# Kernel tuning notes

Measured on AMD Instinct MI355X. Metric: run time of the kernel, lower is better.

Reference implementation:

```python
import jax, jax.numpy as jnp
import numpy as np

N_NODES = 50000
N_EDGES = 600000
N_MOL = 512
N_ATOM_FEAT = 30   # NUMBER_ATOMIC_GRAPH_FEATURES
N_BOND_FEAT = 10   # NUMBER_BOND_GRAPH_FEATURES


def _sh(v):
    # Real solid spherical harmonics l=0..3, e3nn 'component' normalization
    # (sum_m Y_lm^2 = (2l+1) r^{2l}), normalize=False -> homogeneous polynomials.
    x, y, z = v[..., 0], v[..., 1], v[..., 2]
    r2 = x * x + y * y + z * z
    s3, s5, s15, s105 = 3 ** 0.5, 5 ** 0.5, 15 ** 0.5, 105 ** 0.5
    s70_4, s42_4, s7_2, s105_2 = 70 ** 0.5 / 4, 42 ** 0.5 / 4, 7 ** 0.5 / 2, 105 ** 0.5 / 2
    return jnp.stack([
        jnp.ones_like(x),                                               # l=0
        s3 * x, s3 * y, s3 * z,                                         # l=1
        s15 * x * y, s15 * y * z, 0.5 * s5 * (3 * z * z - r2),
        s15 * x * z, 0.5 * s15 * (x * x - y * y),                       # l=2
        s70_4 * y * (3 * x * x - y * y), s105 * x * y * z,
        s42_4 * y * (5 * z * z - r2), s7_2 * z * (5 * z * z - 3 * r2),
        s42_4 * x * (5 * z * z - r2), s105_2 * z * (x * x - y * y),
        s70_4 * x * (x * x - 3 * y * y),                                # l=3 (no TP path uses it)
    ], axis=-1)


def setup_inputs() -> dict:
    key = jax.random.key(0)
    ks = jax.random.split(key, 12)
    positions = jax.random.normal(ks[0], (N_NODES, 3), jnp.float32)
    x = jax.random.normal(ks[1], (N_NODES, N_ATOM_FEAT), jnp.float32)
    edge_attr = jax.random.normal(ks[2], (N_EDGES, N_BOND_FEAT), jnp.float32)
    edge_src = jax.random.randint(ks[3], (N_EDGES,), 0, N_NODES)
    edge_dst = jax.random.randint(ks[4], (N_EDGES,), 0, N_NODES)
    batch = jnp.sort(jax.random.randint(ks[5], (N_NODES,), 0, N_MOL))
    # tp1: FullyConnectedTensorProduct(30x0e, sh) -> live outputs 64x0e + 24x1o + 16x2e
    W1_0 = jax.random.normal(ks[6], (N_ATOM_FEAT, 64), jnp.float32)
    W1_1 = jax.random.normal(ks[7], (N_ATOM_FEAT, 24), jnp.float32)
    W1_2 = jax.random.normal(ks[8], (N_ATOM_FEAT, 16), jnp.float32)
    # tp2: paths 0e*0e, 1o*1o, 2e*2e -> 1x0e
    W2_0 = jax.random.normal(ks[9], (64,), jnp.float32)
    W2_1 = jax.random.normal(ks[10], (24,), jnp.float32)
    W2_2 = jax.random.normal(ks[11], (16,), jnp.float32)
    return dict(positions=positions, x=x, edge_attr=edge_attr,
                W1_0=W1_0, W1_1=W1_1, W1_2=W1_2,
                W2_0=W2_0, W2_1=W2_1, W2_2=W2_2,
                edge_src=edge_src, edge_dst=edge_dst, batch=batch)


def _forward(positions, x, edge_attr, W1_0, W1_1, W1_2, W2_0, W2_1, W2_2,
             edge_src, edge_dst, batch):
    E = edge_src.shape[0]
    seg = jax.ops.segment_sum
    edge_vec = positions[edge_src] - positions[edge_dst]            # [E,3]
    sh = _sh(edge_vec)                                              # [E,16]
    # mul_edges TP: only bond channel 0 has instructions; path_weight sqrt(2l+1)
    # cancels w3j(0,l,l)=I/sqrt(2l+1) exactly -> plain product.
    ea = edge_attr[:, :1] * sh
    ea0, ea1, ea2 = ea[:, 0:1], ea[:, 1:4], ea[:, 4:9]              # l=3 slice unused (no path)
    deg = seg(jnp.ones((E,), sh.dtype), edge_dst, num_segments=N_NODES)
    inv_sqrt_deg = jnp.where(deg > 0, jax.lax.rsqrt(jnp.maximum(deg, 1.0)), 0.0)[:, None]
    # tp1: 0e x l -> l ; path_weight*w3j collapses to 1/sqrt(fan_in=30)
    W1 = jnp.concatenate([W1_0, W1_1, W1_2], axis=1)                # [30,104]
    a = (x[edge_src] @ W1) * (1.0 / np.sqrt(N_ATOM_FEAT))           # [E,104]
    a0, a1, a2 = a[:, :64], a[:, 64:88], a[:, 88:104]
    e_feat = jnp.concatenate([
        a0 * ea0,                                                   # [E,64]  0e
        (a1[:, :, None] * ea1[:, None, :]).reshape(E, 72),          # [E,24*3] 1o
        (a2[:, :, None] * ea2[:, None, :]).reshape(E, 80),          # [E,16*5] 2e
    ], axis=1)                                                      # [E,216]
    n = seg(e_feat, edge_dst, num_segments=N_NODES) * inv_sqrt_deg  # [N,216]
    # tp2: l x l -> 0e, w3j(l,l,0)=I/sqrt(2l+1), path_weight = 1/sqrt(104)
    g = n[edge_src]                                                 # [E,216]
    t0 = (g[:, :64] * ea0) @ W2_0
    t1 = jnp.einsum('eum,em,u->e', g[:, 64:136].reshape(E, 24, 3), ea1, W2_1)
    t2 = jnp.einsum('eum,em,u->e', g[:, 136:216].reshape(E, 16, 5), ea2, W2_2)
    out_e = (t0 + t1 / np.sqrt(3.0) + t2 / np.sqrt(5.0)) * (1.0 / np.sqrt(104.0))
    node = seg(out_e[:, None], edge_dst, num_segments=N_NODES) * inv_sqrt_deg  # [N,1]
    acc = seg(node, batch, num_segments=N_MOL)                      # [M,1]
    atoms = seg(jnp.ones((N_NODES,), node.dtype), batch, num_segments=N_MOL)[:, None]
    return acc * jnp.where(atoms > 0, jax.lax.rsqrt(jnp.maximum(atoms, 1.0)), 0.0)


def reference(positions, x, edge_attr, W1_0, W1_1, W1_2, W2_0, W2_1, W2_2,
              edge_src, edge_dst, batch):
    return _forward(positions, x, edge_attr, W1_0, W1_1, W1_2,
                    W2_0, W2_1, W2_2, edge_src, edge_dst, batch)
```

## Files before the change

### kernel.cpp

```cpp
#include <hip/hip_runtime.h>

#define DEV_INLINE __device__ __forceinline__
#define MAXDEG 48

static DEV_INLINE void sh_l012(float xx, float yy, float zz, float sh[9]) {
    const float s3  = 1.7320508075688772f;
    const float s5  = 2.23606797749979f;
    const float s15 = 3.872983346207417f;
    float r2 = xx * xx + yy * yy + zz * zz;
    sh[0] = 1.0f;
    sh[1] = s3 * xx;
    sh[2] = s3 * yy;
    sh[3] = s3 * zz;
    sh[4] = s15 * xx * yy;
    sh[5] = s15 * yy * zz;
    sh[6] = 0.5f * s5 * (3.0f * zz * zz - r2);
    sh[7] = s15 * xx * zz;
    sh[8] = 0.5f * s15 * (xx * xx - yy * yy);
}

__global__ void k_prep(const float* __restrict__ x,
                       const float* __restrict__ pos,
                       const float* __restrict__ W1_0, const float* __restrict__ W1_1,
                       const float* __restrict__ W1_2, const float* __restrict__ W2_0,
                       const float* __restrict__ W2_1, const float* __restrict__ W2_2,
                       const int* __restrict__ esrc, const int* __restrict__ edst,
                       const float* __restrict__ eattr, const int* __restrict__ batch,
                       float4* __restrict__ node1, float2* __restrict__ node2,
                       int* __restrict__ deg, int2* __restrict__ rec,
                       int* __restrict__ atoms,
                       int n_nodes, int n_edges) {
    __shared__ float ws[90];
    __shared__ int hist[512];
    int t = threadIdx.x;
    int g = blockIdx.x * blockDim.x + t;
    int dst = -1, src_v = 0;
    float ea = 0.f;
    if (g < n_edges) {
        dst = edst[g];
        src_v = esrc[g];
        ea = eattr[(size_t)g * 10];
    }
    bool nodeBlock = (blockIdx.x * blockDim.x) < n_nodes;
    if (nodeBlock) {
        const float inv_s30 = 0.18257418583505536f;
        if (t < 30) {
            float s = 0.f;
            for (int u = 0; u < 64; u++) s += W1_0[t * 64 + u] * W2_0[u];
            ws[t] = s * inv_s30;
        } else if (t < 60) {
            int k = t - 30;
            float s = 0.f;
            for (int u = 0; u < 24; u++) s += W1_1[k * 24 + u] * W2_1[u];
            ws[t] = s * inv_s30;
        } else if (t < 90) {
            int k = t - 60;
            float s = 0.f;
            for (int u = 0; u < 16; u++) s += W1_2[k * 16 + u] * W2_2[u];
            ws[t] = s * inv_s30;
        }
        hist[t] = 0;
        hist[t + 256] = 0;
        __syncthreads();
        if (g < n_nodes) {
            const float* xv = x + (size_t)g * 30;
            float s0 = 0.f, s1 = 0.f, s2 = 0.f;
#pragma unroll
            for (int k = 0; k < 30; k++) {
                float xk = xv[k];
                s0 += xk * ws[k];
                s1 += xk * ws[30 + k];
                s2 += xk * ws[60 + k];
            }
            node1[g] = make_float4(pos[g * 3 + 0], pos[g * 3 + 1], pos[g * 3 + 2], s0);
            node2[g] = make_float2(s1, s2);
        }
        int v0 = blockIdx.x * 256;
        int molFirst = batch[min(v0, n_nodes - 1)];
        if (g < n_nodes) atomicAdd(&hist[batch[g] - molFirst], 1);
        __syncthreads();
        int vend = min(v0 + 255, n_nodes - 1);
        int molLast = batch[vend];
        for (int m = t; m <= molLast - molFirst; m += 256)
            if (hist[m] > 0) atomicAdd(atoms + molFirst + m, hist[m]);
    }
    if (dst >= 0) {
        int r = atomicAdd(deg + dst, 1);
        if (r < MAXDEG) rec[dst * MAXDEG + r] = make_int2(src_v, __float_as_int(ea));
    }
}

__global__ void k_passA(const float4* __restrict__ node1, const float2* __restrict__ node2,
                        const int2* __restrict__ rec, const int* __restrict__ deg,
                        float4* __restrict__ Pkg, float* __restrict__ out,
                        int n_nodes, int n_mol) {
    int g = blockIdx.x * blockDim.x + threadIdx.x;
    if (g < n_mol) out[g] = 0.f;
    int v = g >> 4, r = g & 15;
    if (v >= n_nodes) return;
    int d = min(deg[v], MAXDEG);
    const int2* row = rec + (size_t)v * MAXDEG;
    float4 pv = node1[v];
    float acc[9];
#pragma unroll
    for (int m = 0; m < 9; m++) acc[m] = 0.f;
    for (int i = r; i < d; i += 16) {
        int2 rcd = row[i];
        int src = rcd.x;
        float ea = __int_as_float(rcd.y);
        float4 n1 = node1[src];
        float2 n2 = node2[src];
        float dx = n1.x - pv.x, dy = n1.y - pv.y, dz = n1.z - pv.z;
        float sh[9];
        sh_l012(dx, dy, dz, sh);
        acc[0] += ea * n1.w;
#pragma unroll
        for (int m = 1; m < 4; m++) acc[m] += ea * sh[m] * n2.x;
#pragma unroll
        for (int m = 4; m < 9; m++) acc[m] += ea * sh[m] * n2.y;
    }
#pragma unroll
    for (int off = 1; off < 16; off <<= 1)
#pragma unroll
        for (int m = 0; m < 9; m++) acc[m] += __shfl_xor(acc[m], off);
    if (r == 0) {
        float s = (d > 0) ? rsqrtf((float)d) : 0.f;
        float4* o = Pkg + (size_t)v * 3;
        o[0] = make_float4(acc[0] * s, acc[1] * s, acc[2] * s, acc[3] * s);
        o[1] = make_float4(acc[4] * s, acc[5] * s, acc[6] * s, acc[7] * s);
        o[2] = make_float4(acc[8] * s, pv.x, pv.y, pv.z);
    }
}

__global__ void k_passB(const float4* __restrict__ node1, const float4* __restrict__ Pkg,
                        const int2* __restrict__ rec, const int* __restrict__ deg,
                        const int* __restrict__ batch, const int* __restrict__ atoms,
                        float* __restrict__ out, int n_nodes) {
    __shared__ float smol[512];
    int t = threadIdx.x;
    smol[t] = 0.f;
    smol[t + 256] = 0.f;
    __syncthreads();
    int g = blockIdx.x * blockDim.x + t;
    int v = g >> 4, r = g & 15;
    int v0 = blockIdx.x * 16;
    const float i3 = 0.5773502691896258f;
    const float i5 = 0.4472135954999579f;
    const float i104 = 0.09805806756909202f;
    int molFirst = batch[min(v0, n_nodes - 1)];
    if (v < n_nodes) {
        int d = min(deg[v], MAXDEG);
        const int2* row = rec + (size_t)v * MAXDEG;
        float4 pv = node1[v];
        float s = 0.f;
        for (int i = r; i < d; i += 16) {
            int2 rcd = row[i];
            int src = rcd.x;
            float ea = __int_as_float(rcd.y);
            const float4* Ps = Pkg + (size_t)src * 3;
            float4 p03 = Ps[0];
            float4 p47 = Ps[1];
            float4 p8p = Ps[2];
            float dx = p8p.y - pv.x, dy = p8p.z - pv.y, dz = p8p.w - pv.z;
            float sh[9];
            sh_l012(dx, dy, dz, sh);
            float t1 = sh[1] * p03.y + sh[2] * p03.z + sh[3] * p03.w;
            float t2 = sh[4] * p47.x + sh[5] * p47.y + sh[6] * p47.z + sh[7] * p47.w + sh[8] * p8p.x;
            s += ea * (p03.x + t1 * i3 + t2 * i5);
        }
#pragma unroll
        for (int off = 1; off < 16; off <<= 1) s += __shfl_xor(s, off);
        if (r == 0) {
            float isd = (d > 0) ? rsqrtf((float)d) : 0.f;
            atomicAdd(&smol[batch[v] - molFirst], s * i104 * isd);
        }
    }
    __syncthreads();
    if (v0 < n_nodes) {
        int vend = min(v0 + 15, n_nodes - 1);
        int nm = batch[vend] - molFirst + 1;
        for (int m = t; m < nm; m += 256) {
            float val = smol[m];
            if (val != 0.f) {
                int a = atoms[molFirst + m];
                float inv = (a > 0) ? rsqrtf((float)a) : 0.f;
                atomicAdd(out + molFirst + m, val * inv);
            }
        }
    }
}

extern "C" void kernel_launch(void* const* d_in, const int* in_sizes, int n_in,
                              void* d_out, int out_size, void* d_ws, size_t ws_size,
                              hipStream_t stream) {
    const float* pos   = (const float*)d_in[0];
    const float* x     = (const float*)d_in[1];
    const float* eattr = (const float*)d_in[2];
    const float* W1_0  = (const float*)d_in[3];
    const float* W1_1  = (const float*)d_in[4];
    const float* W1_2  = (const float*)d_in[5];
    const float* W2_0  = (const float*)d_in[6];
    const float* W2_1  = (const float*)d_in[7];
    const float* W2_2  = (const float*)d_in[8];
    const int* esrc  = (const int*)d_in[9];
    const int* edst  = (const int*)d_in[10];
    const int* batch = (const int*)d_in[11];

    const int n_edges = in_sizes[9];
    const int n_nodes = in_sizes[11];
    const int n_mol   = out_size;
    float* out = (float*)d_out;

    const int BS = 256;
    const int NB = (n_nodes + BS - 1) / BS;
    const int EB1 = (n_edges + BS - 1) / BS;
    const int VB16 = (16 * n_nodes + BS - 1) / BS;
    const int GRID1 = (EB1 > NB) ? EB1 : NB;

    char* ws = (char*)d_ws;
    size_t off = 0;
    auto carve = [&](size_t bytes) {
        size_t o = off;
        off = (off + bytes + 255) & ~(size_t)255;
        return o;
    };
    size_t off_deg    = carve((size_t)n_nodes * sizeof(int));
    size_t off_atoms  = carve((size_t)n_mol * sizeof(int));
    size_t zero_bytes = off;
    size_t off_n1     = carve((size_t)n_nodes * sizeof(float4));
    size_t off_n2     = carve((size_t)n_nodes * sizeof(float2));
    size_t off_Pkg    = carve((size_t)n_nodes * 3 * sizeof(float4));
    size_t off_rec    = carve((size_t)n_nodes * MAXDEG * sizeof(int2));
    (void)ws_size;

    int*    deg    = (int*)(ws + off_deg);
    int*    atoms  = (int*)(ws + off_atoms);
    float4* node1  = (float4*)(ws + off_n1);
    float2* node2  = (float2*)(ws + off_n2);
    float4* Pkg    = (float4*)(ws + off_Pkg);
    int2*   rec    = (int2*)(ws + off_rec);

    hipMemsetAsync(d_ws, 0, zero_bytes, stream);

    k_prep<<<GRID1, BS, 0, stream>>>(x, pos, W1_0, W1_1, W1_2, W2_0, W2_1, W2_2,
                                     esrc, edst, eattr, batch,
                                     node1, node2, deg, rec, atoms,
                                     n_nodes, n_edges);
    k_passA<<<VB16, BS, 0, stream>>>(node1, node2, rec, deg, Pkg, out, n_nodes, n_mol);
    k_passB<<<VB16, BS, 0, stream>>>(node1, Pkg, rec, deg, batch, atoms, out, n_nodes);
}
```

Before: 147.2 us.

## Fuse three kernels into one persistent kernel with grid-wide atomic barriers

Replaces the prep, passA and passB launches with a single persistent kernel. It is sized to occupancy times CU count, capped at 2048 blocks, and separates its phases with a software grid barrier built on an atomic counter. Per-molecule atom counts now come from a binary search over the sorted batch array, replacing the shared-memory histogram and atomics. The aim is to remove launch gaps and tail effects between kernels. In exchange it adds spin-barrier overhead, depends on every block being co-resident, and lowers parallelism in the gather passes because threads loop over the work with a grid stride.

```diff
diff --git a/kernel.cpp b/kernel.cpp
--- a/kernel.cpp
+++ b/kernel.cpp
@@ -19,8 +19,192 @@
     sh[8] = 0.5f * s15 * (xx * xx - yy * yy);
 }
 
-__global__ void k_prep(const float* __restrict__ x,
-                       const float* __restrict__ pos,
+static DEV_INLINE int lower_bound_i(const int* __restrict__ a, int n, int key) {
+    int lo = 0, hi = n;
+    while (lo < hi) {
+        int mid = (lo + hi) >> 1;
+        if (a[mid] < key) lo = mid + 1; else hi = mid;
+    }
+    return lo;
+}
+
+static DEV_INLINE void gbar(int* cnt, int nblocks, int phase) {
+    __threadfence();
+    __syncthreads();
+    if (threadIdx.x == 0) {
+        atomicAdd(cnt, 1);
+        const int target = nblocks * phase;
+        int guard = 0;
+        while (atomicAdd(cnt, 0) < target) {
+            __builtin_amdgcn_s_sleep(2);
+            if (++guard > (1 << 27)) break;
+        }
+    }
+    __syncthreads();
+    __threadfence();
+}
+
+__global__ __launch_bounds__(256, 4)
+void k_fused(const float* __restrict__ x, const float* __restrict__ pos,
+             const float* __restrict__ W1_0, const float* __restrict__ W1_1,
+             const float* __restrict__ W1_2, const float* __restrict__ W2_0,
+             const float* __restrict__ W2_1, const float* __restrict__ W2_2,
+             const int* __restrict__ esrc, const int* __restrict__ edst,
+             const float* __restrict__ eattr, const int* __restrict__ batch,
+             float4* __restrict__ node1, float2* __restrict__ node2,
+             int* __restrict__ deg, int2* __restrict__ rec,
+             float* __restrict__ atomsInv, float4* __restrict__ Pkg,
+             float* __restrict__ out, int* __restrict__ barcnt,
+             int n_nodes, int n_edges, int n_mol, int nblocks) {
+    __shared__ float ws[90];
+    __shared__ float smol[512];
+    const int t = threadIdx.x;
+    const int b = blockIdx.x;
+    const int g = b * 256 + t;
+    const int gsz = gridDim.x * 256;
+
+    {
+        const float inv_s30 = 0.18257418583505536f;
+        if (t < 30) {
+            float s = 0.f;
+            for (int u = 0; u < 64; u++) s += W1_0[t * 64 + u] * W2_0[u];
+            ws[t] = s * inv_s30;
+        } else if (t < 60) {
+            int k = t - 30;
+            float s = 0.f;
+            for (int u = 0; u < 24; u++) s += W1_1[k * 24 + u] * W2_1[u];
+            ws[t] = s * inv_s30;
+        } else if (t < 90) {
+            int k = t - 60;
+            float s = 0.f;
+            for (int u = 0; u < 16; u++) s += W1_2[k * 16 + u] * W2_2[u];
+            ws[t] = s * inv_s30;
+        }
+        __syncthreads();
+        for (int v = g; v < n_nodes; v += gsz) {
+            const float* xv = x + (size_t)v * 30;
+            float s0 = 0.f, s1 = 0.f, s2 = 0.f;
+#pragma unroll
+            for (int k = 0; k < 30; k++) {
+                float xk = xv[k];
+                s0 += xk * ws[k];
+                s1 += xk * ws[30 + k];
+                s2 += xk * ws[60 + k];
+            }
+            node1[v] = make_float4(pos[v * 3 + 0], pos[v * 3 + 1], pos[v * 3 + 2], s0);
+            node2[v] = make_float2(s1, s2);
+        }
+        if (b == 0) {
+            for (int m = t; m < n_mol; m += 256) {
+                int lo = lower_bound_i(batch, n_nodes, m);
+                int hi = lower_bound_i(batch, n_nodes, m + 1);
+                int cnt = hi - lo;
+                atomsInv[m] = (cnt > 0) ? rsqrtf((float)cnt) : 0.f;
+                out[m] = 0.f;
+            }
+        }
+    }
+    gbar(barcnt, nblocks, 1);
+
+    for (int e = g; e < n_edges; e += gsz) {
+        int dst = edst[e];
+        int src = esrc[e];
+        float ea = eattr[(size_t)e * 10];
+        int r = atomicAdd(deg + dst, 1);
+        if (r < MAXDEG) rec[(size_t)dst * MAXDEG + r] = make_int2(src, __float_as_int(ea));
+    }
+    gbar(barcnt, nblocks, 2);
+
+    const int total16 = n_nodes * 16;
+    for (int gv = g; gv < total16; gv += gsz) {
+        int v = gv >> 4, r = gv & 15;
+        int d = min(deg[v], MAXDEG);
+        const int2* row = rec + (size_t)v * MAXDEG;
+        float4 pv = node1[v];
+        float acc[9];
+#pragma unroll
+        for (int m = 0; m < 9; m++) acc[m] = 0.f;
+        for (int i = r; i < d; i += 16) {
+            int2 rcd = row[i];
+            int src = rcd.x;
+            float ea = __int_as_float(rcd.y);
+            float4 n1 = node1[src];
+            float2 n2 = node2[src];
+            float dx = n1.x - pv.x, dy = n1.y - pv.y, dz = n1.z - pv.z;
+            float sh[9];
+            sh_l012(dx, dy, dz, sh);
+            acc[0] += ea * n1.w;
+#pragma unroll
+            for (int m = 1; m < 4; m++) acc[m] += ea * sh[m] * n2.x;
+#pragma unroll
+            for (int m = 4; m < 9; m++) acc[m] += ea * sh[m] * n2.y;
+        }
+#pragma unroll
+        for (int off = 1; off < 16; off <<= 1)
+#pragma unroll
+            for (int m = 0; m < 9; m++) acc[m] += __shfl_xor(acc[m], off);
+        if (r == 0) {
+            float s = (d > 0) ? rsqrtf((float)d) : 0.f;
+            float4* o = Pkg + (size_t)v * 3;
+            o[0] = make_float4(acc[0] * s, acc[1] * s, acc[2] * s, acc[3] * s);
+            o[1] = make_float4(acc[4] * s, acc[5] * s, acc[6] * s, acc[7] * s);
+            o[2] = make_float4(acc[8] * s, pv.x, pv.y, pv.z);
+        }
+    }
+    gbar(barcnt, nblocks, 3);
+
+    const float i3 = 0.5773502691896258f;
+    const float i5 = 0.4472135954999579f;
+    const float i104 = 0.09805806756909202f;
+    for (int base = b * 256; base < total16; base += gsz) {
+        int gv = base + t;
+        int v = gv >> 4, r = gv & 15;
+        int v0 = base >> 4;
+        smol[t] = 0.f;
+        smol[t + 256] = 0.f;
+        __syncthreads();
+        int molFirst = batch[min(v0, n_nodes - 1)];
+        if (v < n_nodes) {
+            int d = min(deg[v], MAXDEG);
+            const int2* row = rec + (size_t)v * MAXDEG;
+            float4 pv = node1[v];
+            float s = 0.f;
+            for (int i = r; i < d; i += 16) {
+                int2 rcd = row[i];
+                int src = rcd.x;
+                float ea = __int_as_float(rcd.y);
+                const float4* Ps = Pkg + (size_t)src * 3;
+                float4 p03 = Ps[0];
+                float4 p47 = Ps[1];
+                float4 p8p = Ps[2];
+                float dx = p8p.y - pv.x, dy = p8p.z - pv.y, dz = p8p.w - pv.z;
+                float sh[9];
+                sh_l012(dx, dy, dz, sh);
+                float t1 = sh[1] * p03.y + sh[2] * p03.z + sh[3] * p03.w;
+                float t2 = sh[4] * p47.x + sh[5] * p47.y + sh[6] * p47.z + sh[7] * p47.w + sh[8] * p8p.x;
+                s += ea * (p03.x + t1 * i3 + t2 * i5);
+            }
+#pragma unroll
+            for (int off = 1; off < 16; off <<= 1) s += __shfl_xor(s, off);
+            if (r == 0) {
+                float isd = (d > 0) ? rsqrtf((float)d) : 0.f;
+                atomicAdd(&smol[batch[v] - molFirst], s * i104 * isd);
+            }
+        }
+        __syncthreads();
+        if (v0 < n_nodes) {
+            int vend = min(v0 + 15, n_nodes - 1);
+            int nm = batch[vend] - molFirst + 1;
+            for (int m = t; m < nm; m += 256) {
+                float val = smol[m];
+                if (val != 0.f) atomicAdd(out + molFirst + m, val * atomsInv[molFirst + m]);
+            }
+        }
+        __syncthreads();
+    }
+}
+
+__global__ void k_prep(const float* __restrict__ x, const float* __restrict__ pos,
                        const float* __restrict__ W1_0, const float* __restrict__ W1_1,
                        const float* __restrict__ W1_2, const float* __restrict__ W2_0,
                        const float* __restrict__ W2_1, const float* __restrict__ W2_2,
@@ -28,10 +212,9 @@
                        const float* __restrict__ eattr, const int* __restrict__ batch,
                        float4* __restrict__ node1, float2* __restrict__ node2,
                        int* __restrict__ deg, int2* __restrict__ rec,
-                       int* __restrict__ atoms,
-                       int n_nodes, int n_edges) {
+                       float* __restrict__ atomsInv,
+                       int n_nodes, int n_edges, int n_mol) {
     __shared__ float ws[90];
-    __shared__ int hist[512];
     int t = threadIdx.x;
     int g = blockIdx.x * blockDim.x + t;
     int dst = -1, src_v = 0;
@@ -59,8 +242,6 @@
             for (int u = 0; u < 16; u++) s += W1_2[k * 16 + u] * W2_2[u];
             ws[t] = s * inv_s30;
         }
-        hist[t] = 0;
-        hist[t + 256] = 0;
         __syncthreads();
         if (g < n_nodes) {
             const float* xv = x + (size_t)g * 30;
@@ -75,18 +256,18 @@
             node1[g] = make_float4(pos[g * 3 + 0], pos[g * 3 + 1], pos[g * 3 + 2], s0);
             node2[g] = make_float2(s1, s2);
         }
-        int v0 = blockIdx.x * 256;
-        int molFirst = batch[min(v0, n_nodes - 1)];
-        if (g < n_nodes) atomicAdd(&hist[batch[g] - molFirst], 1);
-        __syncthreads();
-        int vend = min(v0 + 255, n_nodes - 1);
-        int molLast = batch[vend];
-        for (int m = t; m <= molLast - molFirst; m += 256)
-            if (hist[m] > 0) atomicAdd(atoms + molFirst + m, hist[m]);
+    }
+    if (blockIdx.x == 0) {
+        for (int m = t; m < n_mol; m += 256) {
+            int lo = lower_bound_i(batch, n_nodes, m);
+            int hi = lower_bound_i(batch, n_nodes, m + 1);
+            int cnt = hi - lo;
+            atomsInv[m] = (cnt > 0) ? rsqrtf((float)cnt) : 0.f;
+        }
     }
     if (dst >= 0) {
         int r = atomicAdd(deg + dst, 1);
-        if (r < MAXDEG) rec[dst * MAXDEG + r] = make_int2(src_v, __float_as_int(ea));
+        if (r < MAXDEG) rec[(size_t)dst * MAXDEG + r] = make_int2(src_v, __float_as_int(ea));
     }
 }
 
@@ -134,7 +315,7 @@
 
 __global__ void k_passB(const float4* __restrict__ node1, const float4* __restrict__ Pkg,
                         const int2* __restrict__ rec, const int* __restrict__ deg,
-                        const int* __restrict__ batch, const int* __restrict__ atoms,
+                        const int* __restrict__ batch, const float* __restrict__ atomsInv,
                         float* __restrict__ out, int n_nodes) {
     __shared__ float smol[512];
     int t = threadIdx.x;
@@ -181,11 +362,7 @@
         int nm = batch[vend] - molFirst + 1;
         for (int m = t; m < nm; m += 256) {
             float val = smol[m];
-            if (val != 0.f) {
-                int a = atoms[molFirst + m];
-                float inv = (a > 0) ? rsqrtf((float)a) : 0.f;
-                atomicAdd(out + molFirst + m, val * inv);
-            }
+            if (val != 0.f) atomicAdd(out + molFirst + m, val * atomsInv[molFirst + m]);
         }
     }
 }
@@ -206,16 +383,10 @@
     const int* edst  = (const int*)d_in[10];
     const int* batch = (const int*)d_in[11];
 
-    const int n_edges = in_sizes[9];
-    const int n_nodes = in_sizes[11];
-    const int n_mol   = out_size;
+    int n_edges = in_sizes[9];
+    int n_nodes = in_sizes[11];
+    int n_mol   = out_size;
     float* out = (float*)d_out;
-
-    const int BS = 256;
-    const int NB = (n_nodes + BS - 1) / BS;
-    const int EB1 = (n_edges + BS - 1) / BS;
-    const int VB16 = (16 * n_nodes + BS - 1) / BS;
-    const int GRID1 = (EB1 > NB) ? EB1 : NB;
 
     char* ws = (char*)d_ws;
     size_t off = 0;
@@ -224,28 +395,62 @@
         off = (off + bytes + 255) & ~(size_t)255;
         return o;
     };
-    size_t off_deg    = carve((size_t)n_nodes * sizeof(int));
-    size_t off_atoms  = carve((size_t)n_mol * sizeof(int));
+    size_t off_bar  = carve(sizeof(int));
+    size_t off_deg  = carve((size_t)n_nodes * sizeof(int));
     size_t zero_bytes = off;
-    size_t off_n1     = carve((size_t)n_nodes * sizeof(float4));
-    size_t off_n2     = carve((size_t)n_nodes * sizeof(float2));
-    size_t off_Pkg    = carve((size_t)n_nodes * 3 * sizeof(float4));
-    size_t off_rec    = carve((size_t)n_nodes * MAXDEG * sizeof(int2));
+    size_t off_ainv = carve((size_t)n_mol * sizeof(float));
+    size_t off_n1   = carve((size_t)n_nodes * sizeof(float4));
+    size_t off_n2   = carve((size_t)n_nodes * sizeof(float2));
+    size_t off_Pkg  = carve((size_t)n_nodes * 3 * sizeof(float4));
+    size_t off_rec  = carve((size_t)n_nodes * MAXDEG * sizeof(int2));
     (void)ws_size;
 
-    int*    deg    = (int*)(ws + off_deg);
-    int*    atoms  = (int*)(ws + off_atoms);
-    float4* node1  = (float4*)(ws + off_n1);
-    float2* node2  = (float2*)(ws + off_n2);
-    float4* Pkg    = (float4*)(ws + off_Pkg);
-    int2*   rec    = (int2*)(ws + off_rec);
+    int*    barcnt   = (int*)(ws + off_bar);
+    int*    deg      = (int*)(ws + off_deg);
+    float*  atomsInv = (float*)(ws + off_ainv);
+    float4* node1    = (float4*)(ws + off_n1);
+    float2* node2    = (float2*)(ws + off_n2);
+    float4* Pkg      = (float4*)(ws + off_Pkg);
+    int2*   rec      = (int2*)(ws + off_rec);
+
+    static int g_blocks = 0;
+    if (g_blocks == 0) {
+        int occ = 0;
+        hipError_t e1 = hipOccupancyMaxActiveBlocksPerMultiprocessor(
+            &occ, (const void*)k_fused, 256, 0);
+        int dev = 0;
+        hipGetDevice(&dev);
+        hipDeviceProp_t props;
+        hipError_t e2 = hipGetDeviceProperties(&props, dev);
+        if (e1 == hipSuccess && e2 == hipSuccess && occ >= 1 &&
+            props.multiProcessorCount >= 1) {
+            long long cap = (long long)occ * props.multiProcessorCount;
+            if (cap > 2048) cap = 2048;
+            g_blocks = (int)cap;
+        } else {
+            g_blocks = -1;
+        }
+    }
 
     hipMemsetAsync(d_ws, 0, zero_bytes, stream);
 
-    k_prep<<<GRID1, BS, 0, stream>>>(x, pos, W1_0, W1_1, W1_2, W2_0, W2_1, W2_2,
-                                     esrc, edst, eattr, batch,
-                                     node1, node2, deg, rec, atoms,
-                                     n_nodes, n_edges);
-    k_passA<<<VB16, BS, 0, stream>>>(node1, node2, rec, deg, Pkg, out, n_nodes, n_mol);
-    k_passB<<<VB16, BS, 0, stream>>>(node1, Pkg, rec, deg, batch, atoms, out, n_nodes);
-}
+    if (g_blocks > 0) {
+        k_fused<<<g_blocks, 256, 0, stream>>>(
+            x, pos, W1_0, W1_1, W1_2, W2_0, W2_1, W2_2,
+            esrc, edst, eattr, batch,
+            node1, node2, deg, rec, atomsInv, Pkg, out, barcnt,
+            n_nodes, n_edges, n_mol, g_blocks);
+    } else {
+        const int BS = 256;
+        const int EB1 = (n_edges + BS - 1) / BS;
+        const int NB  = (n_nodes + BS - 1) / BS;
+        const int GRID1 = (EB1 > NB) ? EB1 : NB;
+        const int VB16 = (16 * n_nodes + BS - 1) / BS;
+        k_prep<<<GRID1, BS, 0, stream>>>(x, pos, W1_0, W1_1, W1_2, W2_0, W2_1, W2_2,
+                                         esrc, edst, eattr, batch,
+                                         node1, node2, deg, rec, atomsInv,
+                                         n_nodes, n_edges, n_mol);
+        k_passA<<<VB16, BS, 0, stream>>>(node1, node2, rec, deg, Pkg, out, n_nodes, n_mol);
+        k_passB<<<VB16, BS, 0, stream>>>(node1, Pkg, rec, deg, batch, atomsInv, out, n_nodes);
+    }
+}
```

Measured after the change: 504.6 us. +242.7%, slower.

## Fuse both message passes by recomputing neighbor aggregates and pack edge records

Applied to the files above, without the earlier changes.

Drops the intermediate per-node package buffer and the separate first pass. The second pass now recomputes each source node's 9-component aggregate from that node's own neighbor list, for every incoming edge. Edge records shrink to 32 bits: a 16-bit source index plus an fp16 edge attribute. Molecule atom counts are now found by binary search over the sorted batch array in one block, instead of shared-memory histograms. The aim is to save a launch and the package-buffer traffic, but the two-hop recompute multiplies the inner edge work by roughly the average degree. The 16-bit index and fp16 attribute also limit node count and precision.

```diff
diff --git a/kernel.cpp b/kernel.cpp
--- a/kernel.cpp
+++ b/kernel.cpp
@@ -1,7 +1,22 @@
 #include <hip/hip_runtime.h>
+#include <hip/hip_fp16.h>
 
 #define DEV_INLINE __device__ __forceinline__
 #define MAXDEG 48
+
+static DEV_INLINE unsigned pack_rec(int src, float ea) {
+    __half h = __float2half(ea);
+    unsigned short bits;
+    __builtin_memcpy(&bits, &h, 2);
+    return ((unsigned)src << 16) | (unsigned)bits;
+}
+static DEV_INLINE int rec_src(unsigned rcd) { return (int)(rcd >> 16); }
+static DEV_INLINE float rec_ea(unsigned rcd) {
+    unsigned short bits = (unsigned short)(rcd & 0xFFFFu);
+    __half h;
+    __builtin_memcpy(&h, &bits, 2);
+    return __half2float(h);
+}
 
 static DEV_INLINE void sh_l012(float xx, float yy, float zz, float sh[9]) {
     const float s3  = 1.7320508075688772f;
@@ -19,19 +34,26 @@
     sh[8] = 0.5f * s15 * (xx * xx - yy * yy);
 }
 
-__global__ void k_prep(const float* __restrict__ x,
-                       const float* __restrict__ pos,
+static DEV_INLINE int lower_bound_i(const int* __restrict__ a, int n, int key) {
+    int lo = 0, hi = n;
+    while (lo < hi) {
+        int mid = (lo + hi) >> 1;
+        if (a[mid] < key) lo = mid + 1; else hi = mid;
+    }
+    return lo;
+}
+
+__global__ void k_prep(const float* __restrict__ x, const float* __restrict__ pos,
                        const float* __restrict__ W1_0, const float* __restrict__ W1_1,
                        const float* __restrict__ W1_2, const float* __restrict__ W2_0,
                        const float* __restrict__ W2_1, const float* __restrict__ W2_2,
                        const int* __restrict__ esrc, const int* __restrict__ edst,
                        const float* __restrict__ eattr, const int* __restrict__ batch,
                        float4* __restrict__ node1, float2* __restrict__ node2,
-                       int* __restrict__ deg, int2* __restrict__ rec,
-                       int* __restrict__ atoms,
-                       int n_nodes, int n_edges) {
+                       int* __restrict__ deg, unsigned* __restrict__ rec,
+                       float* __restrict__ atomsInv, float* __restrict__ out,
+                       int n_nodes, int n_edges, int n_mol) {
     __shared__ float ws[90];
-    __shared__ int hist[512];
     int t = threadIdx.x;
     int g = blockIdx.x * blockDim.x + t;
     int dst = -1, src_v = 0;
@@ -59,8 +81,6 @@
             for (int u = 0; u < 16; u++) s += W1_2[k * 16 + u] * W2_2[u];
             ws[t] = s * inv_s30;
         }
-        hist[t] = 0;
-        hist[t + 256] = 0;
         __syncthreads();
         if (g < n_nodes) {
             const float* xv = x + (size_t)g * 30;
@@ -75,67 +95,26 @@
             node1[g] = make_float4(pos[g * 3 + 0], pos[g * 3 + 1], pos[g * 3 + 2], s0);
             node2[g] = make_float2(s1, s2);
         }
-        int v0 = blockIdx.x * 256;
-        int molFirst = batch[min(v0, n_nodes - 1)];
-        if (g < n_nodes) atomicAdd(&hist[batch[g] - molFirst], 1);
-        __syncthreads();
-        int vend = min(v0 + 255, n_nodes - 1);
-        int molLast = batch[vend];
-        for (int m = t; m <= molLast - molFirst; m += 256)
-            if (hist[m] > 0) atomicAdd(atoms + molFirst + m, hist[m]);
+    }
+    if (blockIdx.x == 0) {
+        for (int m = t; m < n_mol; m += 256) {
+            int lo = lower_bound_i(batch, n_nodes, m);
+            int hi = lower_bound_i(batch, n_nodes, m + 1);
+            int cnt = hi - lo;
+            atomsInv[m] = (cnt > 0) ? rsqrtf((float)cnt) : 0.f;
+            out[m] = 0.f;
+        }
     }
     if (dst >= 0) {
         int r = atomicAdd(deg + dst, 1);
-        if (r < MAXDEG) rec[dst * MAXDEG + r] = make_int2(src_v, __float_as_int(ea));
-    }
-}
-
-__global__ void k_passA(const float4* __restrict__ node1, const float2* __restrict__ node2,
-                        const int2* __restrict__ rec, const int* __restrict__ deg,
-                        float4* __restrict__ Pkg, float* __restrict__ out,
-                        int n_nodes, int n_mol) {
-    int g = blockIdx.x * blockDim.x + threadIdx.x;
-    if (g < n_mol) out[g] = 0.f;
-    int v = g >> 4, r = g & 15;
-    if (v >= n_nodes) return;
-    int d = min(deg[v], MAXDEG);
-    const int2* row = rec + (size_t)v * MAXDEG;
-    float4 pv = node1[v];
-    float acc[9];
-#pragma unroll
-    for (int m = 0; m < 9; m++) acc[m] = 0.f;
-    for (int i = r; i < d; i += 16) {
-        int2 rcd = row[i];
-        int src = rcd.x;
-        float ea = __int_as_float(rcd.y);
-        float4 n1 = node1[src];
-        float2 n2 = node2[src];
-        float dx = n1.x - pv.x, dy = n1.y - pv.y, dz = n1.z - pv.z;
-        float sh[9];
-        sh_l012(dx, dy, dz, sh);
-        acc[0] += ea * n1.w;
-#pragma unroll
-        for (int m = 1; m < 4; m++) acc[m] += ea * sh[m] * n2.x;
-#pragma unroll
-        for (int m = 4; m < 9; m++) acc[m] += ea * sh[m] * n2.y;
-    }
-#pragma unroll
-    for (int off = 1; off < 16; off <<= 1)
-#pragma unroll
-        for (int m = 0; m < 9; m++) acc[m] += __shfl_xor(acc[m], off);
-    if (r == 0) {
-        float s = (d > 0) ? rsqrtf((float)d) : 0.f;
-        float4* o = Pkg + (size_t)v * 3;
-        o[0] = make_float4(acc[0] * s, acc[1] * s, acc[2] * s, acc[3] * s);
-        o[1] = make_float4(acc[4] * s, acc[5] * s, acc[6] * s, acc[7] * s);
-        o[2] = make_float4(acc[8] * s, pv.x, pv.y, pv.z);
-    }
-}
-
-__global__ void k_passB(const float4* __restrict__ node1, const float4* __restrict__ Pkg,
-                        const int2* __restrict__ rec, const int* __restrict__ deg,
-                        const int* __restrict__ batch, const int* __restrict__ atoms,
-                        float* __restrict__ out, int n_nodes) {
+        if (r < MAXDEG) rec[(size_t)dst * MAXDEG + r] = pack_rec(src_v, ea);
+    }
+}
+
+__global__ void k_msg(const float4* __restrict__ node1, const float2* __restrict__ node2,
+                      const unsigned* __restrict__ rec, const int* __restrict__ deg,
+                      const int* __restrict__ batch, const float* __restrict__ atomsInv,
+                      float* __restrict__ out, int n_nodes) {
     __shared__ float smol[512];
     int t = threadIdx.x;
     smol[t] = 0.f;
@@ -150,23 +129,42 @@
     int molFirst = batch[min(v0, n_nodes - 1)];
     if (v < n_nodes) {
         int d = min(deg[v], MAXDEG);
-        const int2* row = rec + (size_t)v * MAXDEG;
+        const unsigned* row = rec + (size_t)v * MAXDEG;
         float4 pv = node1[v];
         float s = 0.f;
         for (int i = r; i < d; i += 16) {
-            int2 rcd = row[i];
-            int src = rcd.x;
-            float ea = __int_as_float(rcd.y);
-            const float4* Ps = Pkg + (size_t)src * 3;
-            float4 p03 = Ps[0];
-            float4 p47 = Ps[1];
-            float4 p8p = Ps[2];
-            float dx = p8p.y - pv.x, dy = p8p.z - pv.y, dz = p8p.w - pv.z;
+            unsigned rcd = row[i];
+            int src = rec_src(rcd);
+            float ea = rec_ea(rcd);
+            int d2 = min(deg[src], MAXDEG);
+            const unsigned* row2 = rec + (size_t)src * MAXDEG;
+            float4 ps = node1[src];
+            float acc[9];
+#pragma unroll
+            for (int m = 0; m < 9; m++) acc[m] = 0.f;
+            for (int j = 0; j < d2; j++) {
+                unsigned r2 = row2[j];
+                int s2 = rec_src(r2);
+                float ea2 = rec_ea(r2);
+                float4 n1 = node1[s2];
+                float2 n2 = node2[s2];
+                float dx = n1.x - ps.x, dy = n1.y - ps.y, dz = n1.z - ps.z;
+                float sh[9];
+                sh_l012(dx, dy, dz, sh);
+                acc[0] += ea2 * n1.w;
+#pragma unroll
+                for (int m = 1; m < 4; m++) acc[m] += ea2 * sh[m] * n2.x;
+#pragma unroll
+                for (int m = 4; m < 9; m++) acc[m] += ea2 * sh[m] * n2.y;
+            }
+            float isd_s = (d2 > 0) ? rsqrtf((float)d2) : 0.f;
+            float dx = ps.x - pv.x, dy = ps.y - pv.y, dz = ps.z - pv.z;
             float sh[9];
             sh_l012(dx, dy, dz, sh);
-            float t1 = sh[1] * p03.y + sh[2] * p03.z + sh[3] * p03.w;
-            float t2 = sh[4] * p47.x + sh[5] * p47.y + sh[6] * p47.z + sh[7] * p47.w + sh[8] * p8p.x;
-            s += ea * (p03.x + t1 * i3 + t2 * i5);
+            float t1 = sh[1] * acc[1] + sh[2] * acc[2] + sh[3] * acc[3];
+            float t2 = sh[4] * acc[4] + sh[5] * acc[5] + sh[6] * acc[6] +
+                       sh[7] * acc[7] + sh[8] * acc[8];
+            s += ea * isd_s * (acc[0] + t1 * i3 + t2 * i5);
         }
 #pragma unroll
         for (int off = 1; off < 16; off <<= 1) s += __shfl_xor(s, off);
@@ -181,11 +179,7 @@
         int nm = batch[vend] - molFirst + 1;
         for (int m = t; m < nm; m += 256) {
             float val = smol[m];
-            if (val != 0.f) {
-                int a = atoms[molFirst + m];
-                float inv = (a > 0) ? rsqrtf((float)a) : 0.f;
-                atomicAdd(out + molFirst + m, val * inv);
-            }
+            if (val != 0.f) atomicAdd(out + molFirst + m, val * atomsInv[molFirst + m]);
         }
     }
 }
@@ -225,27 +219,25 @@
         return o;
     };
     size_t off_deg    = carve((size_t)n_nodes * sizeof(int));
-    size_t off_atoms  = carve((size_t)n_mol * sizeof(int));
     size_t zero_bytes = off;
+    size_t off_ainv   = carve((size_t)n_mol * sizeof(float));
     size_t off_n1     = carve((size_t)n_nodes * sizeof(float4));
     size_t off_n2     = carve((size_t)n_nodes * sizeof(float2));
-    size_t off_Pkg    = carve((size_t)n_nodes * 3 * sizeof(float4));
-    size_t off_rec    = carve((size_t)n_nodes * MAXDEG * sizeof(int2));
+    size_t off_rec    = carve((size_t)n_nodes * MAXDEG * sizeof(unsigned));
     (void)ws_size;
 
-    int*    deg    = (int*)(ws + off_deg);
-    int*    atoms  = (int*)(ws + off_atoms);
-    float4* node1  = (float4*)(ws + off_n1);
-    float2* node2  = (float2*)(ws + off_n2);
-    float4* Pkg    = (float4*)(ws + off_Pkg);
-    int2*   rec    = (int2*)(ws + off_rec);
+    int*      deg      = (int*)(ws + off_deg);
+    float*    atomsInv = (float*)(ws + off_ainv);
+    float4*   node1    = (float4*)(ws + off_n1);
+    float2*   node2    = (float2*)(ws + off_n2);
+    unsigned* rec      = (unsigned*)(ws + off_rec);
 
     hipMemsetAsync(d_ws, 0, zero_bytes, stream);
 
     k_prep<<<GRID1, BS, 0, stream>>>(x, pos, W1_0, W1_1, W1_2, W2_0, W2_1, W2_2,
                                      esrc, edst, eattr, batch,
-                                     node1, node2, deg, rec, atoms,
-                                     n_nodes, n_edges);
-    k_passA<<<VB16, BS, 0, stream>>>(node1, node2, rec, deg, Pkg, out, n_nodes, n_mol);
-    k_passB<<<VB16, BS, 0, stream>>>(node1, Pkg, rec, deg, batch, atoms, out, n_nodes);
-}
+                                     node1, node2, deg, rec, atomsInv, out,
+                                     n_nodes, n_edges, n_mol);
+    k_msg<<<VB16, BS, 0, stream>>>(node1, node2, rec, deg, batch, atomsInv,
+                                   out, n_nodes);
+}
```

New measurement: 254.7 us. 73.0% more time.
